# Optimization experiments

Measured on AMD Instinct MI355X. Metric: run time of the kernel, lower is better.

## Reference

```python
import jax, jax.numpy as jnp
import numpy as np


def setup_inputs() -> dict:
    key = jax.random.key(0)
    ks = jax.random.split(key, 9)
    B, C, H, W, D = 2, 64, 64, 64, 16
    Cq = C // 8
    return {
        "x2d": jax.random.normal(ks[0], (B, C, H, W, D), jnp.float32),
        "x3d": jax.random.normal(ks[1], (B, C, H, W, D), jnp.float32),
        "Wq": jax.random.normal(ks[2], (Cq, C), jnp.float32) * 0.05,
        "bq": jax.random.normal(ks[3], (Cq,), jnp.float32) * 0.05,
        "Wk": jax.random.normal(ks[4], (Cq, C), jnp.float32) * 0.05,
        "bk": jax.random.normal(ks[5], (Cq,), jnp.float32) * 0.05,
        "Wv": jax.random.normal(ks[6], (C, C), jnp.float32) * 0.05,
        "bv": jax.random.normal(ks[7], (C,), jnp.float32) * 0.05,
        "gamma": jax.random.normal(ks[8], (1,), jnp.float32),
    }


def reference(x2d, x3d, Wq, bq, Wk, bk, Wv, bv, gamma):
    # x2d/x3d: (B, C, H, W, D) -> permute to (B, C, D, H, W)
    xp = jnp.transpose(x2d, (0, 1, 4, 2, 3))
    B, C, D, H, W = xp.shape
    N = H * W

    # 1x1x1 Conv3d == channel contraction
    q = jnp.einsum('oc,bcdhw->bodhw', Wq, xp) + bq[None, :, None, None, None]
    k = jnp.einsum('oc,bcdhw->bodhw', Wk, xp) + bk[None, :, None, None, None]
    v = jnp.einsum('oc,bcdhw->bodhw', Wv, xp) + bv[None, :, None, None, None]

    # fold depth into feature dim; attention over N = H*W positions
    pq = q.reshape(B, -1, N)                  # (B, Cq*D, N)
    pk = k.reshape(B, -1, N)                  # (B, Cq*D, N)
    energy = jnp.einsum('bcn,bcm->bnm', pq, pk)   # (B, N, N)
    attn = jax.nn.softmax(energy, axis=-1)

    pv = v.reshape(B, -1, N)                  # (B, C*D, N)
    # out[b,c,n] = sum_m pv[b,c,m] * attn[b,n,m]
    out = jnp.einsum('bcm,bnm->bcn', pv, attn)
    out = out.reshape(B, C, D, H, W)
    out = jnp.transpose(out, (0, 1, 3, 4, 2))  # back to (B, C, H, W, D)
    return gamma * out + x3d
```

## Files before the change

### kernel.cpp

```cpp
#include <hip/hip_runtime.h>
#include <hip/hip_bf16.h>

typedef __attribute__((ext_vector_type(8)))  __bf16 bf16x8;
typedef __attribute__((ext_vector_type(4)))  float  f32x4;
typedef __attribute__((ext_vector_type(16))) float  f32x16;

#define N_   4096
#define CQD  128

static __device__ __forceinline__ unsigned short f2bf(float f) {
    union { float f; unsigned int u; } cv; cv.f = f;
    unsigned int u = cv.u;
    u += 0x7fffu + ((u >> 16) & 1u);
    return (unsigned short)(u >> 16);
}
static __device__ __forceinline__ f32x4 mfma16(bf16x8 a, bf16x8 b, f32x4 c) {
    return __builtin_amdgcn_mfma_f32_16x16x32_bf16(a, b, c, 0, 0, 0);
}
static __device__ __forceinline__ f32x16 mfma32(bf16x8 a, bf16x8 b, f32x16 c) {
    return __builtin_amdgcn_mfma_f32_32x32x16_bf16(a, b, c, 0, 0, 0);
}

__global__ __launch_bounds__(256) void proj_kernel(
    const float* __restrict__ x2d,
    const float* __restrict__ Wq, const float* __restrict__ bq,
    const float* __restrict__ Wk, const float* __restrict__ bk,
    const float* __restrict__ Wv, const float* __restrict__ bv,
    unsigned short* __restrict__ Qb, unsigned short* __restrict__ Kb,
    unsigned short* __restrict__ PV)
{
    const int t    = threadIdx.x;
    const int blk  = blockIdx.x;
    const int b    = blk >> 8;
    const int tile = blk & 255;
    const int col  = (tile << 8) + t;
    const int n    = col >> 4;
    const int dd   = col & 15;
    const int lane = t & 63;

    const float* xb = x2d + (size_t)b * 64 * 65536 + col;
    float xr[64];
#pragma unroll
    for (int c = 0; c < 64; ++c) xr[c] = xb[(size_t)c * 65536];

    unsigned short* qb  = Qb + (size_t)b * N_ * CQD + (size_t)n * CQD + dd;
    unsigned short* kb  = Kb + (size_t)b * N_ * CQD + (size_t)n * CQD + dd;
    unsigned short* pvb = PV + (size_t)b * 1024 * N_;

    auto wptr = [&](int jb) -> const float* {
        if (jb < 8)  return Wq + jb * 64;
        if (jb < 16) return Wk + (jb - 8) * 64;
        return Wv + (jb - 16) * 64;
    };
    auto bptr = [&](int jb) -> const float* {
        if (jb < 8)  return bq + jb;
        if (jb < 16) return bk + (jb - 8);
        return bv + (jb - 16);
    };

    float wc[4], wn[4];
    {
        const float* wp = wptr(0);
#pragma unroll
        for (int jj = 0; jj < 4; ++jj) wc[jj] = wp[jj * 64 + lane];
    }
    for (int jc = 0; jc < 20; ++jc) {
        const int jb = jc * 4;
        {
            const float* wp = wptr(jb + 4 < 80 ? jb + 4 : 0);
#pragma unroll
            for (int jj = 0; jj < 4; ++jj) wn[jj] = wp[jj * 64 + lane];
        }
        const float* bp = bptr(jb);
        float acc[4];
#pragma unroll
        for (int jj = 0; jj < 4; ++jj) acc[jj] = bp[jj];
#pragma unroll
        for (int c = 0; c < 64; ++c) {
#pragma unroll
            for (int jj = 0; jj < 4; ++jj) {
                const float wv_ = __int_as_float(
                    __builtin_amdgcn_readlane(__float_as_int(wc[jj]), c));
                acc[jj] += wv_ * xr[c];
            }
        }
        if (jb < 8) {
#pragma unroll
            for (int jj = 0; jj < 4; ++jj) qb[(jb + jj) * 16] = f2bf(acc[jj]);
        } else if (jb < 16) {
#pragma unroll
            for (int jj = 0; jj < 4; ++jj) kb[(jb - 8 + jj) * 16] = f2bf(acc[jj]);
        } else {
#pragma unroll
            for (int jj = 0; jj < 4; ++jj)
                pvb[(size_t)(((jb - 16 + jj) << 4) + dd) * N_ + n] = f2bf(acc[jj]);
        }
#pragma unroll
        for (int jj = 0; jj < 4; ++jj) wc[jj] = wn[jj];
    }
}

__global__ __launch_bounds__(512, 2) void attn_kernel(
    const unsigned short* __restrict__ Qb, const unsigned short* __restrict__ Kb,
    const unsigned short* __restrict__ PV,
    const float* __restrict__ x3d, const float* __restrict__ gamma_p,
    float* __restrict__ outp)
{
    __shared__ __align__(16) unsigned char p_lds[2][8192];
    __shared__ float red[64];

    const int t   = threadIdx.x;
    const int w   = t >> 6;
    const int l   = t & 63;
    const int lo  = l & 15;
    const int hi  = l >> 4;
    const int lo5 = l & 31;
    const int hi1 = l >> 5;

    const int id    = blockIdx.x;
    const int combo = id & 3;
    const int ch    = combo & 1;
    const int b     = combo >> 1;
    const int ntile = id >> 2;
    const int n0    = ntile << 6;
    const int msel  = w & 3;
    const int nh    = w >> 2;
    const int cb    = (ch << 9) + (w << 6);

    const unsigned short* qp  = Qb + (size_t)b * N_ * CQD;
    const unsigned short* kp  = Kb + (size_t)b * N_ * CQD;
    const unsigned short* pvp = PV + (size_t)b * 1024 * N_;

    bf16x8 qf[2][4];
#pragma unroll
    for (int nb = 0; nb < 2; ++nb)
#pragma unroll
        for (int kk = 0; kk < 4; ++kk)
            qf[nb][kk] = *reinterpret_cast<const bf16x8*>(
                qp + (size_t)(n0 + nh * 32 + nb * 16 + lo) * CQD + kk * 32 + hi * 8);

    bf16x8 kc[4];
#pragma unroll
    for (int kk = 0; kk < 4; ++kk)
        kc[kk] = *reinterpret_cast<const bf16x8*>(
            kp + (size_t)(msel * 16 + lo) * CQD + kk * 32 + hi * 8);

    f32x16 acc[2][2];
#pragma unroll
    for (int i = 0; i < 2; ++i)
#pragma unroll
        for (int j = 0; j < 2; ++j)
#pragma unroll
            for (int r = 0; r < 16; ++r) acc[i][j][r] = 0.f;
    float rs[2] = {0.f, 0.f};

    if (t < 64) red[t] = 0.f;

    for (int it = 0; it < 64; ++it) {
        const int m0 = it << 6;

        bf16x8 Bf[4][2];
#pragma unroll
        for (int ms = 0; ms < 4; ++ms)
#pragma unroll
            for (int cs = 0; cs < 2; ++cs)
                Bf[ms][cs] = *reinterpret_cast<const bf16x8*>(
                    pvp + (size_t)(cb + cs * 32 + lo5) * N_ + m0 + ms * 16 + hi1 * 8);
        const int mnext = (it < 63) ? (m0 + 64) : 0;
        bf16x8 kn[4];
#pragma unroll
        for (int kk = 0; kk < 4; ++kk)
            kn[kk] = *reinterpret_cast<const bf16x8*>(
                kp + (size_t)(mnext + msel * 16 + lo) * CQD + kk * 32 + hi * 8);

        f32x4 e[2];
#pragma unroll
        for (int nb = 0; nb < 2; ++nb) e[nb] = (f32x4){0.f, 0.f, 0.f, 0.f};
#pragma unroll
        for (int kk = 0; kk < 4; ++kk)
#pragma unroll
            for (int nb = 0; nb < 2; ++nb)
                e[nb] = mfma16(kc[kk], qf[nb][kk], e[nb]);

        unsigned char* pb = p_lds[it & 1];
#pragma unroll
        for (int nb = 0; nb < 2; ++nb) {
            const int row  = nh * 32 + nb * 16 + lo;
            const int cswz = (((msel * 2 + (hi >> 1)) ^ (row & 7)) << 4) + (hi & 1) * 8;
#pragma unroll
            for (int s = 0; s < 2; ++s) {
                const float p0 = __expf(e[nb][2 * s]);
                const float p1 = __expf(e[nb][2 * s + 1]);
                rs[nb] += p0 + p1;
                const unsigned int pk = ((unsigned int)f2bf(p1) << 16) | f2bf(p0);
                *reinterpret_cast<unsigned int*>(pb + row * 128 + cswz + s * 4) = pk;
            }
        }
        __syncthreads();

#pragma unroll
        for (int ms = 0; ms < 4; ++ms) {
            bf16x8 pa[2];
#pragma unroll
            for (int nb = 0; nb < 2; ++nb) {
                const int row = nb * 32 + lo5;
                pa[nb] = *reinterpret_cast<const bf16x8*>(
                    pb + row * 128 + (((ms * 2 + hi1) ^ (row & 7)) << 4));
            }
#pragma unroll
            for (int nb = 0; nb < 2; ++nb)
#pragma unroll
                for (int cs = 0; cs < 2; ++cs)
                    acc[nb][cs] = mfma32(pa[nb], Bf[ms][cs], acc[nb][cs]);
        }
#pragma unroll
        for (int kk = 0; kk < 4; ++kk) kc[kk] = kn[kk];
    }

#pragma unroll
    for (int nb = 0; nb < 2; ++nb) {
        float v = rs[nb];
        v += __shfl_xor(v, 16);
        v += __shfl_xor(v, 32);
        rs[nb] = v;
    }
    if (l < 16) {
        atomicAdd(&red[nh * 32 + l],      rs[0]);
        atomicAdd(&red[nh * 32 + 16 + l], rs[1]);
    }
    __syncthreads();

    const float gmv  = gamma_p[0];
    const float* x3p = x3d + (size_t)b * 64 * 65536;
    float*       op  = outp + (size_t)b * 64 * 65536;
#pragma unroll
    for (int nb = 0; nb < 2; ++nb) {
#pragma unroll
        for (int j = 0; j < 16; ++j) {
            const int   nl   = nb * 32 + hi1 * 4 + (j & 3) + ((j >> 2) * 8);
            const float rinv = 1.0f / red[nl];
            const int   nn   = n0 + nl;
#pragma unroll
            for (int cs = 0; cs < 2; ++cs) {
                const int    cp  = cb + cs * 32 + lo5;
                const size_t idx = (size_t)(cp >> 4) * 65536 + (size_t)nn * 16 + (cp & 15);
                op[idx] = gmv * acc[nb][cs][j] * rinv + x3p[idx];
            }
        }
    }
}

extern "C" void kernel_launch(void* const* d_in, const int* in_sizes, int n_in,
                              void* d_out, int out_size, void* d_ws, size_t ws_size,
                              hipStream_t stream)
{
    const float* x2d = (const float*)d_in[0];
    const float* x3d = (const float*)d_in[1];
    const float* Wq  = (const float*)d_in[2];
    const float* bq  = (const float*)d_in[3];
    const float* Wk  = (const float*)d_in[4];
    const float* bk  = (const float*)d_in[5];
    const float* Wv  = (const float*)d_in[6];
    const float* bv  = (const float*)d_in[7];
    const float* gm  = (const float*)d_in[8];

    char* ws = (char*)d_ws;
    unsigned short* Qb = (unsigned short*)ws;
    unsigned short* Kb = (unsigned short*)(ws + (2u << 20));
    unsigned short* PV = (unsigned short*)(ws + (4u << 20));

    proj_kernel<<<512, 256, 0, stream>>>(x2d, Wq, bq, Wk, bk, Wv, bv, Qb, Kb, PV);
    attn_kernel<<<256, 512, 0, stream>>>(Qb, Kb, PV, x3d, gm, (float*)d_out);
}
```

Baseline: 336.0 us.

## Store K and V in MFMA fragment layout and stream PV via global_load_lds

The projection kernel now stages Q, K and V tiles in shared memory and writes K and V into a pre-swizzled fragment layout, so the attention kernel can load them with contiguous 16-byte accesses. The attention kernel is restructured to 512 blocks, each covering a quarter of the channels. It double-buffers V tiles directly into LDS with global_load_lds, uses 32-wide key steps over 128 iterations, and raises occupancy to 4 blocks per CU. The goal is to remove strided PV global loads and improve latency hiding. In exchange it adds a barrier per iteration and recomputes the QK energy once per channel quarter.

```diff
diff --git a/kernel.cpp b/kernel.cpp
--- a/kernel.cpp
+++ b/kernel.cpp
@@ -5,8 +5,7 @@
 typedef __attribute__((ext_vector_type(4)))  float  f32x4;
 typedef __attribute__((ext_vector_type(16))) float  f32x16;
 
-#define N_   4096
-#define CQD  128
+#define N_ 4096
 
 static __device__ __forceinline__ unsigned short f2bf(float f) {
     union { float f; unsigned int u; } cv; cv.f = f;
@@ -21,92 +20,103 @@
     return __builtin_amdgcn_mfma_f32_32x32x16_bf16(a, b, c, 0, 0, 0);
 }
 
+
 __global__ __launch_bounds__(256) void proj_kernel(
     const float* __restrict__ x2d,
     const float* __restrict__ Wq, const float* __restrict__ bq,
     const float* __restrict__ Wk, const float* __restrict__ bk,
     const float* __restrict__ Wv, const float* __restrict__ bv,
-    unsigned short* __restrict__ Qb, unsigned short* __restrict__ Kb,
-    unsigned short* __restrict__ PV)
+    unsigned short* __restrict__ Qb, unsigned short* __restrict__ KF,
+    unsigned short* __restrict__ PVF)
 {
+    __shared__ unsigned short vlds[1024][16];
+    __shared__ unsigned short qlds[16][128];
+    __shared__ unsigned short klds[16][128];
+
     const int t    = threadIdx.x;
     const int blk  = blockIdx.x;
     const int b    = blk >> 8;
     const int tile = blk & 255;
     const int col  = (tile << 8) + t;
-    const int n    = col >> 4;
     const int dd   = col & 15;
-    const int lane = t & 63;
+    const int ml   = (col >> 4) & 15;
+    const int mt   = tile >> 1;
+    const int mq   = tile & 1;
 
     const float* xb = x2d + (size_t)b * 64 * 65536 + col;
     float xr[64];
 #pragma unroll
     for (int c = 0; c < 64; ++c) xr[c] = xb[(size_t)c * 65536];
 
-    unsigned short* qb  = Qb + (size_t)b * N_ * CQD + (size_t)n * CQD + dd;
-    unsigned short* kb  = Kb + (size_t)b * N_ * CQD + (size_t)n * CQD + dd;
-    unsigned short* pvb = PV + (size_t)b * 1024 * N_;
-
-    auto wptr = [&](int jb) -> const float* {
-        if (jb < 8)  return Wq + jb * 64;
-        if (jb < 16) return Wk + (jb - 8) * 64;
-        return Wv + (jb - 16) * 64;
-    };
-    auto bptr = [&](int jb) -> const float* {
-        if (jb < 8)  return bq + jb;
-        if (jb < 16) return bk + (jb - 8);
-        return bv + (jb - 16);
-    };
-
-    float wc[4], wn[4];
-    {
-        const float* wp = wptr(0);
-#pragma unroll
-        for (int jj = 0; jj < 4; ++jj) wc[jj] = wp[jj * 64 + lane];
-    }
-    for (int jc = 0; jc < 20; ++jc) {
-        const int jb = jc * 4;
-        {
-            const float* wp = wptr(jb + 4 < 80 ? jb + 4 : 0);
-#pragma unroll
-            for (int jj = 0; jj < 4; ++jj) wn[jj] = wp[jj * 64 + lane];
-        }
-        const float* bp = bptr(jb);
-        float acc[4];
-#pragma unroll
-        for (int jj = 0; jj < 4; ++jj) acc[jj] = bp[jj];
-#pragma unroll
+    {
+        float aq[8], ak[8];
+#pragma unroll
+        for (int j = 0; j < 8; ++j) { aq[j] = bq[j]; ak[j] = bk[j]; }
+#pragma unroll 8
         for (int c = 0; c < 64; ++c) {
-#pragma unroll
-            for (int jj = 0; jj < 4; ++jj) {
-                const float wv_ = __int_as_float(
-                    __builtin_amdgcn_readlane(__float_as_int(wc[jj]), c));
-                acc[jj] += wv_ * xr[c];
+            const float xv = xr[c];
+#pragma unroll
+            for (int j = 0; j < 8; ++j) {
+                aq[j] += Wq[j * 64 + c] * xv;
+                ak[j] += Wk[j * 64 + c] * xv;
             }
         }
-        if (jb < 8) {
-#pragma unroll
-            for (int jj = 0; jj < 4; ++jj) qb[(jb + jj) * 16] = f2bf(acc[jj]);
-        } else if (jb < 16) {
-#pragma unroll
-            for (int jj = 0; jj < 4; ++jj) kb[(jb - 8 + jj) * 16] = f2bf(acc[jj]);
-        } else {
-#pragma unroll
-            for (int jj = 0; jj < 4; ++jj)
-                pvb[(size_t)(((jb - 16 + jj) << 4) + dd) * N_ + n] = f2bf(acc[jj]);
-        }
-#pragma unroll
-        for (int jj = 0; jj < 4; ++jj) wc[jj] = wn[jj];
-    }
-}
-
-__global__ __launch_bounds__(512, 2) void attn_kernel(
-    const unsigned short* __restrict__ Qb, const unsigned short* __restrict__ Kb,
-    const unsigned short* __restrict__ PV,
+#pragma unroll
+        for (int j = 0; j < 8; ++j) {
+            qlds[ml][j * 16 + dd] = f2bf(aq[j]);
+            klds[ml][j * 16 + dd] = f2bf(ak[j]);
+        }
+    }
+#pragma unroll 1
+    for (int jc = 0; jc < 16; ++jc) {
+        float av[4];
+#pragma unroll
+        for (int jj = 0; jj < 4; ++jj) av[jj] = bv[jc * 4 + jj];
+#pragma unroll 8
+        for (int c = 0; c < 64; ++c) {
+            const float xv = xr[c];
+#pragma unroll
+            for (int jj = 0; jj < 4; ++jj) av[jj] += Wv[(jc * 4 + jj) * 64 + c] * xv;
+        }
+#pragma unroll
+        for (int jj = 0; jj < 4; ++jj)
+            vlds[(jc * 4 + jj) * 16 + dd][ml] = f2bf(av[jj]);
+    }
+    __syncthreads();
+
+    {
+        const int row = t >> 4, slot = t & 15;
+        const uint4 qv = *reinterpret_cast<const uint4*>(&qlds[row][slot << 3]);
+        unsigned short* qd = Qb + (size_t)b * 524288 + ((size_t)((tile << 4) + row) << 7) + (slot << 3);
+        *reinterpret_cast<uint4*>(qd) = qv;
+    }
+    {
+        const int kk = t >> 6, hh = (t >> 4) & 3, ll = t & 15;
+        const uint4 kv = *reinterpret_cast<const uint4*>(&klds[ll][(kk << 5) + (hh << 3)]);
+        unsigned short* kd = KF + (size_t)b * 524288 + ((size_t)(mt << 1) + mq) * 2048 + (t << 3);
+        *reinterpret_cast<uint4*>(kd) = kv;
+    }
+    {
+        unsigned short* pvt = PVF + (size_t)b * 4194304 + (size_t)mt * 32768;
+        const int cblk = t >> 3;
+        const int hi1  = (t >> 2) & 1;
+#pragma unroll
+        for (int j = 0; j < 8; ++j) {
+            const int lo5 = ((t & 3) << 3) + j;
+            const uint4 vv = *reinterpret_cast<const uint4*>(&vlds[(cblk << 5) + lo5][hi1 << 3]);
+            *reinterpret_cast<uint4*>(&pvt[(cblk << 10) + (mq << 9) + (hi1 << 8) + (lo5 << 3)]) = vv;
+        }
+    }
+}
+
+__global__ __launch_bounds__(512, 4) void attn_kernel(
+    const unsigned short* __restrict__ Qb, const unsigned short* __restrict__ KF,
+    const unsigned short* __restrict__ PVF,
     const float* __restrict__ x3d, const float* __restrict__ gamma_p,
     float* __restrict__ outp)
 {
-    __shared__ __align__(16) unsigned char p_lds[2][8192];
+    __shared__ __align__(16) unsigned short pvlds[2][8192];
+    __shared__ __align__(16) unsigned short plds[2048];
     __shared__ float red[64];
 
     const int t   = threadIdx.x;
@@ -114,138 +124,123 @@
     const int l   = t & 63;
     const int lo  = l & 15;
     const int hi  = l >> 4;
-    const int lo5 = l & 31;
-    const int hi1 = l >> 5;
+    const int l8  = l << 3;
 
     const int id    = blockIdx.x;
-    const int combo = id & 3;
-    const int ch    = combo & 1;
-    const int b     = combo >> 1;
-    const int ntile = id >> 2;
-    const int n0    = ntile << 6;
-    const int msel  = w & 3;
-    const int nh    = w >> 2;
-    const int cb    = (ch << 9) + (w << 6);
-
-    const unsigned short* qp  = Qb + (size_t)b * N_ * CQD;
-    const unsigned short* kp  = Kb + (size_t)b * N_ * CQD;
-    const unsigned short* pvp = PV + (size_t)b * 1024 * N_;
-
-    bf16x8 qf[2][4];
-#pragma unroll
-    for (int nb = 0; nb < 2; ++nb)
+    const int combo = id & 7;
+    const int b     = combo >> 2;
+    const int cq    = combo & 3;
+    const int n0    = (id >> 3) << 6;
+    const int mq    = w >> 2;
+    const int ng    = w & 3;
+    const int nh    = w & 1;
+    const int cg    = w >> 1;
+
+    const unsigned short* qp   = Qb  + (size_t)b * 524288;
+    const unsigned short* kfp  = KF  + (size_t)b * 524288;
+    const unsigned short* pvfp = PVF + (size_t)b * 4194304;
+
+    bf16x8 qf[4];
+#pragma unroll
+    for (int kk = 0; kk < 4; ++kk)
+        qf[kk] = *reinterpret_cast<const bf16x8*>(
+            qp + ((size_t)(n0 + ng * 16 + lo) << 7) + (kk << 5) + (hi << 3));
+
+    bf16x8 kc[4], kcn[4];
+#pragma unroll
+    for (int kk = 0; kk < 4; ++kk)
+        kc[kk] = *reinterpret_cast<const bf16x8*>(kfp + (size_t)mq * 2048 + (kk << 9) + l8);
+#pragma unroll
+    for (int r2 = 0; r2 < 2; ++r2) {
+        const int round = (w << 1) + r2;
+        __builtin_amdgcn_global_load_lds(
+            (const __attribute__((address_space(1))) void*)(pvfp + (cq << 13) + (round << 9) + l8),
+            (__attribute__((address_space(3))) void*)(&pvlds[0][round << 9]),
+            16, 0, 0);
+    }
+
+    f32x16 acc[2];
+#pragma unroll
+    for (int cs = 0; cs < 2; ++cs)
+#pragma unroll
+        for (int r = 0; r < 16; ++r) acc[cs][r] = 0.f;
+    float rs = 0.f;
+    if (t < 64) red[t] = 0.f;
+
+    for (int it = 0; it < 128; ++it) {
+        const int cur = it & 1;
+        __syncthreads();
+
+        const int mtn = (it < 127) ? it + 1 : 127;
+        const unsigned short* srcb = pvfp + (size_t)mtn * 32768 + (cq << 13);
+#pragma unroll
+        for (int r2 = 0; r2 < 2; ++r2) {
+            const int round = (w << 1) + r2;
+            __builtin_amdgcn_global_load_lds(
+                (const __attribute__((address_space(1))) void*)(srcb + (round << 9) + l8),
+                (__attribute__((address_space(3))) void*)(&pvlds[cur ^ 1][round << 9]),
+                16, 0, 0);
+        }
+        const unsigned short* kfb = kfp + ((size_t)(mtn << 1) + mq) * 2048;
 #pragma unroll
         for (int kk = 0; kk < 4; ++kk)
-            qf[nb][kk] = *reinterpret_cast<const bf16x8*>(
-                qp + (size_t)(n0 + nh * 32 + nb * 16 + lo) * CQD + kk * 32 + hi * 8);
-
-    bf16x8 kc[4];
-#pragma unroll
-    for (int kk = 0; kk < 4; ++kk)
-        kc[kk] = *reinterpret_cast<const bf16x8*>(
-            kp + (size_t)(msel * 16 + lo) * CQD + kk * 32 + hi * 8);
-
-    f32x16 acc[2][2];
-#pragma unroll
-    for (int i = 0; i < 2; ++i)
-#pragma unroll
-        for (int j = 0; j < 2; ++j)
-#pragma unroll
-            for (int r = 0; r < 16; ++r) acc[i][j][r] = 0.f;
-    float rs[2] = {0.f, 0.f};
-
-    if (t < 64) red[t] = 0.f;
-
-    for (int it = 0; it < 64; ++it) {
-        const int m0 = it << 6;
-
-        bf16x8 Bf[4][2];
-#pragma unroll
-        for (int ms = 0; ms < 4; ++ms)
-#pragma unroll
-            for (int cs = 0; cs < 2; ++cs)
-                Bf[ms][cs] = *reinterpret_cast<const bf16x8*>(
-                    pvp + (size_t)(cb + cs * 32 + lo5) * N_ + m0 + ms * 16 + hi1 * 8);
-        const int mnext = (it < 63) ? (m0 + 64) : 0;
-        bf16x8 kn[4];
-#pragma unroll
-        for (int kk = 0; kk < 4; ++kk)
-            kn[kk] = *reinterpret_cast<const bf16x8*>(
-                kp + (size_t)(mnext + msel * 16 + lo) * CQD + kk * 32 + hi * 8);
-
-        f32x4 e[2];
-#pragma unroll
-        for (int nb = 0; nb < 2; ++nb) e[nb] = (f32x4){0.f, 0.f, 0.f, 0.f};
-#pragma unroll
-        for (int kk = 0; kk < 4; ++kk)
-#pragma unroll
-            for (int nb = 0; nb < 2; ++nb)
-                e[nb] = mfma16(kc[kk], qf[nb][kk], e[nb]);
-
-        unsigned char* pb = p_lds[it & 1];
-#pragma unroll
-        for (int nb = 0; nb < 2; ++nb) {
-            const int row  = nh * 32 + nb * 16 + lo;
-            const int cswz = (((msel * 2 + (hi >> 1)) ^ (row & 7)) << 4) + (hi & 1) * 8;
-#pragma unroll
-            for (int s = 0; s < 2; ++s) {
-                const float p0 = __expf(e[nb][2 * s]);
-                const float p1 = __expf(e[nb][2 * s + 1]);
-                rs[nb] += p0 + p1;
-                const unsigned int pk = ((unsigned int)f2bf(p1) << 16) | f2bf(p0);
-                *reinterpret_cast<unsigned int*>(pb + row * 128 + cswz + s * 4) = pk;
+            kcn[kk] = *reinterpret_cast<const bf16x8*>(kfb + (kk << 9) + l8);
+
+        f32x4 e = (f32x4){0.f, 0.f, 0.f, 0.f};
+#pragma unroll
+        for (int kk = 0; kk < 4; ++kk) e = mfma16(kc[kk], qf[kk], e);
+
+        const float p0 = __expf(e[0]), p1 = __expf(e[1]);
+        const float p2 = __expf(e[2]), p3 = __expf(e[3]);
+        rs += (p0 + p1) + (p2 + p3);
+        const unsigned int w0 = ((unsigned int)f2bf(p1) << 16) | f2bf(p0);
+        const unsigned int w1 = ((unsigned int)f2bf(p3) << 16) | f2bf(p2);
+        const int u = ((ng >> 1) << 7) + (mq << 6) + ((hi >> 1) << 5) + ((ng & 1) << 4) + lo;
+        *reinterpret_cast<uint2*>(&plds[(u << 3) + ((hi & 1) << 2)]) = make_uint2(w0, w1);
+
+        asm volatile("s_waitcnt lgkmcnt(0)" ::: "memory");
+        __builtin_amdgcn_sched_barrier(0);
+        __builtin_amdgcn_s_barrier();
+        __builtin_amdgcn_sched_barrier(0);
+
+        const unsigned short* pvc = &pvlds[cur][0];
+#pragma unroll
+        for (int ks = 0; ks < 2; ++ks) {
+            const bf16x8 pa = *reinterpret_cast<const bf16x8*>(&plds[(nh << 10) + (ks << 9) + l8]);
+#pragma unroll
+            for (int cs = 0; cs < 2; ++cs) {
+                const int cblk = (cg << 1) + cs;
+                const bf16x8 Bf = *reinterpret_cast<const bf16x8*>(&pvc[(cblk << 10) + (ks << 9) + l8]);
+                acc[cs] = mfma32(pa, Bf, acc[cs]);
             }
         }
-        __syncthreads();
-
-#pragma unroll
-        for (int ms = 0; ms < 4; ++ms) {
-            bf16x8 pa[2];
-#pragma unroll
-            for (int nb = 0; nb < 2; ++nb) {
-                const int row = nb * 32 + lo5;
-                pa[nb] = *reinterpret_cast<const bf16x8*>(
-                    pb + row * 128 + (((ms * 2 + hi1) ^ (row & 7)) << 4));
-            }
-#pragma unroll
-            for (int nb = 0; nb < 2; ++nb)
-#pragma unroll
-                for (int cs = 0; cs < 2; ++cs)
-                    acc[nb][cs] = mfma32(pa[nb], Bf[ms][cs], acc[nb][cs]);
-        }
-#pragma unroll
-        for (int kk = 0; kk < 4; ++kk) kc[kk] = kn[kk];
-    }
-
-#pragma unroll
-    for (int nb = 0; nb < 2; ++nb) {
-        float v = rs[nb];
+#pragma unroll
+        for (int kk = 0; kk < 4; ++kk) kc[kk] = kcn[kk];
+    }
+
+    {
+        float v = rs;
         v += __shfl_xor(v, 16);
         v += __shfl_xor(v, 32);
-        rs[nb] = v;
-    }
-    if (l < 16) {
-        atomicAdd(&red[nh * 32 + l],      rs[0]);
-        atomicAdd(&red[nh * 32 + 16 + l], rs[1]);
+        if (l < 16) atomicAdd(&red[ng * 16 + l], v);
     }
     __syncthreads();
 
     const float gmv  = gamma_p[0];
+    const int   lo5  = l & 31;
+    const int   hi1  = l >> 5;
     const float* x3p = x3d + (size_t)b * 64 * 65536;
     float*       op  = outp + (size_t)b * 64 * 65536;
 #pragma unroll
-    for (int nb = 0; nb < 2; ++nb) {
+    for (int cs = 0; cs < 2; ++cs) {
+        const int    cp   = cq * 256 + cg * 64 + cs * 32 + lo5;
+        const size_t base = (size_t)(cp >> 4) * 65536 + (size_t)(cp & 15);
 #pragma unroll
         for (int j = 0; j < 16; ++j) {
-            const int   nl   = nb * 32 + hi1 * 4 + (j & 3) + ((j >> 2) * 8);
+            const int   nl   = nh * 32 + (j & 3) + ((j >> 2) << 3) + (hi1 << 2);
             const float rinv = 1.0f / red[nl];
-            const int   nn   = n0 + nl;
-#pragma unroll
-            for (int cs = 0; cs < 2; ++cs) {
-                const int    cp  = cb + cs * 32 + lo5;
-                const size_t idx = (size_t)(cp >> 4) * 65536 + (size_t)nn * 16 + (cp & 15);
-                op[idx] = gmv * acc[nb][cs][j] * rinv + x3p[idx];
-            }
+            const size_t idx = base + (size_t)(n0 + nl) * 16;
+            op[idx] = gmv * acc[cs][j] * rinv + x3p[idx];
         }
     }
 }
@@ -265,10 +260,10 @@
     const float* gm  = (const float*)d_in[8];
 
     char* ws = (char*)d_ws;
-    unsigned short* Qb = (unsigned short*)ws;
-    unsigned short* Kb = (unsigned short*)(ws + (2u << 20));
-    unsigned short* PV = (unsigned short*)(ws + (4u << 20));
-
-    proj_kernel<<<512, 256, 0, stream>>>(x2d, Wq, bq, Wk, bk, Wv, bv, Qb, Kb, PV);
-    attn_kernel<<<256, 512, 0, stream>>>(Qb, Kb, PV, x3d, gm, (float*)d_out);
-}
+    unsigned short* Qb  = (unsigned short*)ws;
+    unsigned short* KF  = (unsigned short*)(ws + (2u << 20));
+    unsigned short* PVF = (unsigned short*)(ws + (4u << 20));
+
+    proj_kernel<<<512, 256, 0, stream>>>(x2d, Wq, bq, Wk, bk, Wv, bv, Qb, KF, PVF);
+    attn_kernel<<<512, 512, 0, stream>>>(Qb, KF, PVF, x3d, gm, (float*)d_out);
+}
```

Result: no change. 329.5 us (-1.9%).
